# Optimization experiments

Measured on AMD Instinct MI355X. Metric: run time of the kernel, lower is better.

## Reference

```python
import jax, jax.numpy as jnp
from jax import lax
import numpy as np

# db6 decomposition low-pass filter (pywt convention)
_DB6_DEC_LO = np.array([
    -0.00107730108499558, 0.004777257511010651, 0.0005538422009938016,
    -0.031582039318031156, 0.02752286553001629, 0.09750160558707936,
    -0.12976686756709563, -0.22626469396516913, 0.3152503517092432,
    0.7511339080215775, 0.4946238903983854, 0.11154074335008017], dtype=np.float64)

def _make_filters():
    dec_lo = _DB6_DEC_LO
    rec_lo = dec_lo[::-1].copy()
    rec_hi = rec_lo[::-1].copy(); rec_hi[1::2] *= -1.0   # qmf(rec_lo)
    dec_hi = rec_hi[::-1].copy()
    # analysis implemented as correlation -> use time-reversed dec filters (= rec filters)
    a_lo = jnp.asarray(rec_lo, jnp.float32); a_hi = jnp.asarray(rec_hi, jnp.float32)
    # synthesis (conv_transpose) == correlation with flipped rec filters (= dec filters)
    s_lo = jnp.asarray(dec_lo, jnp.float32); s_hi = jnp.asarray(dec_hi, jnp.float32)
    return a_lo, a_hi, s_lo, s_hi

A_LO, A_HI, S_LO, S_HI = _make_filters()
FLEN = 12  # db6 filter length
LEVEL = 3

def _afb_last(x):
    """Analysis filter bank along last axis: symmetric pad + stride-2 correlation.
    x: [B,C,H,W] -> (lo, hi) each [B,C,H,outsize], outsize = floor((W+L-1)/2)."""
    B, C, H, W = x.shape
    outsize = (W + FLEN - 1) // 2
    p = 2 * (outsize - 1) - W + FLEN
    xp = jnp.pad(x, ((0, 0), (0, 0), (0, 0), (p // 2, (p + 1) // 2)), mode='symmetric')
    xr = xp.reshape(B * C * H, 1, xp.shape[-1])
    k = jnp.stack([A_LO, A_HI])[:, None, :]          # (2,1,L)
    y = lax.conv_general_dilated(xr, k, (2,), 'VALID')  # (BCH, 2, outsize)
    y = y.reshape(B, C, H, 2, outsize)
    return y[..., 0, :], y[..., 1, :]

def _sfb_last(lo, hi):
    """Synthesis filter bank along last axis via zero-upsampling + correlation.
    lo, hi: [B,C,H,n] -> [B,C,H,2n+2-L] (matches conv_transpose(stride=2, padding=L-2))."""
    B, C, H, n = lo.shape
    x2 = jnp.concatenate([lo.reshape(B * C * H, 1, n), hi.reshape(B * C * H, 1, n)], axis=1)
    k = jnp.stack([S_LO, S_HI])[None, :, :]          # (1,2,L)
    y = lax.conv_general_dilated(x2, k, (1,), [(1, 1)], lhs_dilation=(2,))
    return y.reshape(B, C, H, 2 * n + 2 - FLEN)

def _dwt2d(x):
    lo, hi = _afb_last(x)                            # along width
    llT, lhT = _afb_last(lo.swapaxes(-1, -2))        # along height
    hlT, hhT = _afb_last(hi.swapaxes(-1, -2))
    ll = llT.swapaxes(-1, -2)
    yh = jnp.stack([lhT.swapaxes(-1, -2), hlT.swapaxes(-1, -2), hhT.swapaxes(-1, -2)], axis=-1)
    return ll, yh                                    # ll [B,C,h,w], yh [B,C,h,w,3]

def _idwt2d(ll, yh):
    lh, hl, hh = yh[..., 0], yh[..., 1], yh[..., 2]
    ll = ll[..., :lh.shape[-2], :lh.shape[-1]]       # crop coarse ll to match highs
    lo = _sfb_last(ll.swapaxes(-1, -2), lh.swapaxes(-1, -2)).swapaxes(-1, -2)
    hi = _sfb_last(hl.swapaxes(-1, -2), hh.swapaxes(-1, -2)).swapaxes(-1, -2)
    return _sfb_last(lo, hi)

def _interp_bilinear(w, out_hw):
    """F.interpolate(mode='bilinear', align_corners=False) on [I,O,h,w] weights."""
    I, O, h, wd = w.shape
    Ho, Wo = int(out_hw[0]), int(out_hw[1])
    if (h, wd) == (Ho, Wo):
        return w
    ys = jnp.clip((jnp.arange(Ho, dtype=jnp.float32) + 0.5) * (h / Ho) - 0.5, 0.0, h - 1.0)
    xs = jnp.clip((jnp.arange(Wo, dtype=jnp.float32) + 0.5) * (wd / Wo) - 0.5, 0.0, wd - 1.0)
    y0 = jnp.floor(ys).astype(jnp.int32); y1 = jnp.minimum(y0 + 1, h - 1)
    x0 = jnp.floor(xs).astype(jnp.int32); x1 = jnp.minimum(x0 + 1, wd - 1)
    ty = (ys - y0)[:, None]; tx = xs - x0
    g = lambda yi, xi: w[:, :, yi, :][:, :, :, xi]
    top = g(y0, x0) * (1 - tx) + g(y0, x1) * tx
    bot = g(y1, x0) * (1 - tx) + g(y1, x1) * tx
    return top * (1 - ty) + bot * ty

def reference(x, weights):
    ll = x
    yh = []
    for _ in range(LEVEL):
        ll, h = _dwt2d(ll)
        yh.append(h)
    out_ll = jnp.einsum('bixy,ioxy->boxy', ll, _interp_bilinear(weights, ll.shape[-2:]))
    out_yh = [jnp.einsum('bixyz,ioxy->boxyz', h, _interp_bilinear(weights, h.shape[2:4])) for h in yh]
    y = out_ll
    for h in reversed(out_yh):
        y = _idwt2d(y, h)
    return y[:, :, :x.shape[2], :x.shape[3]]

def setup_inputs() -> dict:
    key = jax.random.key(0)
    k1, k2 = jax.random.split(key)
    B, Cin, Cout, H, W = 8, 64, 64, 256, 256
    x = jax.random.normal(k1, (B, Cin, H, W), dtype=jnp.float32)
    scale = 1.0 / (Cin * Cout)
    weights = scale * jax.random.uniform(k2, (Cin, Cout, 64, 64), dtype=jnp.float32)
    return {"x": x, "weights": weights}
```

## Files before the change

kernel.cpp:

```cpp
#include <hip/hip_runtime.h>

#define D0  -0.00107730108499558f
#define D1   0.004777257511010651f
#define D2   0.0005538422009938016f
#define D3  -0.031582039318031156f
#define D4   0.02752286553001629f
#define D5   0.09750160558707936f
#define D6  -0.12976686756709563f
#define D7  -0.22626469396516913f
#define D8   0.3152503517092432f
#define D9   0.7511339080215775f
#define D10  0.4946238903983854f
#define D11  0.11154074335008017f

__constant__ float c_ALO[12] = { D11, D10, D9, D8, D7, D6, D5, D4, D3, D2, D1, D0 };
__constant__ float c_AHI[12] = { D0, -D1, D2, -D3, D4, -D5, D6, -D7, D8, -D9, D10, -D11 };
__constant__ float c_SLO[12] = { D0, D1, D2, D3, D4, D5, D6, D7, D8, D9, D10, D11 };
__constant__ float c_SHI[12] = { -D11, D10, -D9, D8, -D7, D6, -D5, D4, -D3, D2, -D1, D0 };

#define NB 512

__device__ __forceinline__ void fma4(float4& a, const float4 v, const float c) {
  a.x = fmaf(v.x, c, a.x); a.y = fmaf(v.y, c, a.y);
  a.z = fmaf(v.z, c, a.z); a.w = fmaf(v.w, c, a.w);
}


__global__ __launch_bounds__(256) void k_afb_rows_nchw(
    const float* __restrict__ x, float4* __restrict__ lo, float4* __restrict__ hi) {
  __shared__ float lds[32][257];
  int h = blockIdx.x >> 4;
  int n0 = (blockIdx.x & 15) << 5;
  for (int idx = threadIdx.x; idx < 32 * 64; idx += 256) {
    int r = idx >> 6, c4 = idx & 63;
    float4 v = *(const float4*)(x + ((long)(n0 + r) * 256 + h) * 256 + (c4 << 2));
    int c = c4 << 2;
    lds[r][c] = v.x; lds[r][c + 1] = v.y; lds[r][c + 2] = v.z; lds[r][c + 3] = v.w;
  }
  __syncthreads();
  int nl4 = threadIdx.x & 7;
  int r0 = nl4 << 2;
  for (int k = threadIdx.x >> 3; k < 133; k += 32) {
    int base = 2 * k - 10;
    float4 aL = {0, 0, 0, 0}, aH = {0, 0, 0, 0};
#pragma unroll
    for (int t = 0; t < 12; ++t) {
      int j = base + t;
      j = (j < 0) ? (-j - 1) : ((j >= 256) ? (511 - j) : j);
      float v0 = lds[r0][j], v1 = lds[r0 + 1][j], v2 = lds[r0 + 2][j], v3 = lds[r0 + 3][j];
      float cl = c_ALO[t], ch = c_AHI[t];
      aL.x = fmaf(v0, cl, aL.x); aL.y = fmaf(v1, cl, aL.y);
      aL.z = fmaf(v2, cl, aL.z); aL.w = fmaf(v3, cl, aL.w);
      aH.x = fmaf(v0, ch, aH.x); aH.y = fmaf(v1, ch, aH.y);
      aH.z = fmaf(v2, ch, aH.z); aH.w = fmaf(v3, ch, aH.w);
    }
    long ob = ((long)h * 133 + k) * 128 + (n0 >> 2) + nl4;
    lo[ob] = aL;
    hi[ob] = aH;
  }
}

__global__ __launch_bounds__(256) void k_afb_rows_cl(
    const float4* __restrict__ in, float4* __restrict__ lo, float4* __restrict__ hi,
    int Win, int outW, int padL, int total) {
  int half = threadIdx.x >> 7, lane = threadIdx.x & 127;
  int p = blockIdx.x * 2 + half;
  if (p >= total) return;
  int h = p / outW, k = p - h * outW;
  int base = 2 * k - padL;
  const float4* rowb = in + (long)h * Win * 128;
  float4 aL = {0, 0, 0, 0}, aH = {0, 0, 0, 0};
#pragma unroll
  for (int t = 0; t < 12; ++t) {
    int j = base + t;
    j = (j < 0) ? (-j - 1) : ((j >= Win) ? (2 * Win - 1 - j) : j);
    float4 v = rowb[(long)j * 128 + lane];
    fma4(aL, v, c_ALO[t]);
    fma4(aH, v, c_AHI[t]);
  }
  long ob = (long)p * 128 + lane;
  lo[ob] = aL;
  hi[ob] = aH;
}

__global__ __launch_bounds__(256) void k_afb_cols_cl(
    const float4* __restrict__ in, float4* __restrict__ lo, float4* __restrict__ hi,
    int Hin, int W, int padL, int total) {
  int half = threadIdx.x >> 7, lane = threadIdx.x & 127;
  int p = blockIdx.x * 2 + half;
  if (p >= total) return;
  int k = p / W, w = p - k * W;
  int base = 2 * k - padL;
  long rstride = (long)W * 128;
  const float4* colb = in + (long)w * 128;
  float4 aL = {0, 0, 0, 0}, aH = {0, 0, 0, 0};
#pragma unroll
  for (int t = 0; t < 12; ++t) {
    int j = base + t;
    j = (j < 0) ? (-j - 1) : ((j >= Hin) ? (2 * Hin - 1 - j) : j);
    float4 v = colb[(long)j * rstride + lane];
    fma4(aL, v, c_ALO[t]);
    fma4(aH, v, c_AHI[t]);
  }
  long ob = (long)p * 128 + lane;
  lo[ob] = aL;
  hi[ob] = aH;
}


__global__ __launch_bounds__(256) void k_sfb_cols_cl(
    const float4* __restrict__ lo, long lors, const float4* __restrict__ hi, long hirs,
    float4* __restrict__ out, int n, int W, int total) {
  int half = threadIdx.x >> 7, lane = threadIdx.x & 127;
  int p = blockIdx.x * 2 + half;
  if (p >= total) return;
  int m = p / W, w = p - m * W;
  int t0 = 1 - (m & 1);
  const float4* lob = lo + (long)w * 128;
  const float4* hib = hi + (long)w * 128;
  float4 acc = {0, 0, 0, 0};
#pragma unroll
  for (int s6 = 0; s6 < 6; ++s6) {
    int t = t0 + 2 * s6;
    int j = (m + t - 1) >> 1;
    if (j >= 0 && j < n) {
      fma4(acc, lob[(long)j * lors + lane], c_SLO[t]);
      fma4(acc, hib[(long)j * hirs + lane], c_SHI[t]);
    }
  }
  out[(long)p * 128 + lane] = acc;
}

__global__ __launch_bounds__(256) void k_sfb_rows_cl(
    const float4* __restrict__ lo, long lors, const float4* __restrict__ hi, long hirs,
    float4* __restrict__ out, int n, int outW, int total) {
  int half = threadIdx.x >> 7, lane = threadIdx.x & 127;
  int p = blockIdx.x * 2 + half;
  if (p >= total) return;
  int h = p / outW, m = p - h * outW;
  int t0 = 1 - (m & 1);
  const float4* lob = lo + (long)h * lors;
  const float4* hib = hi + (long)h * hirs;
  float4 acc = {0, 0, 0, 0};
#pragma unroll
  for (int s6 = 0; s6 < 6; ++s6) {
    int t = t0 + 2 * s6;
    int j = (m + t - 1) >> 1;
    if (j >= 0 && j < n) {
      fma4(acc, lob[(long)j * 128 + lane], c_SLO[t]);
      fma4(acc, hib[(long)j * 128 + lane], c_SHI[t]);
    }
  }
  out[(long)p * 128 + lane] = acc;
}

__global__ __launch_bounds__(256) void k_sfb_rows_to_nchw(
    const float4* __restrict__ lo, const float4* __restrict__ hi, float4* __restrict__ out) {
  __shared__ float lds[32 * 257];
  int h = blockIdx.x >> 3;
  int m0 = (blockIdx.x & 7) << 5;
  const float4* lob = lo + (long)h * 133 * 128;
  const float4* hib = hi + (long)h * 133 * 128;
  for (int c = 0; c < 2; ++c) {
    int n04 = c << 6;
    for (int idx = threadIdx.x; idx < 32 * 64; idx += 256) {
      int ml = idx >> 6, nl4 = idx & 63;
      int m = m0 + ml;
      int t0 = 1 - (m & 1);
      float4 acc = {0, 0, 0, 0};
#pragma unroll
      for (int s6 = 0; s6 < 6; ++s6) {
        int t = t0 + 2 * s6;
        int j = (m + t - 1) >> 1;
        if (j >= 0 && j < 133) {
          fma4(acc, lob[(long)j * 128 + n04 + nl4], c_SLO[t]);
          fma4(acc, hib[(long)j * 128 + n04 + nl4], c_SHI[t]);
        }
      }
      int cb = ml * 257 + (nl4 << 2);
      lds[cb] = acc.x; lds[cb + 1] = acc.y; lds[cb + 2] = acc.z; lds[cb + 3] = acc.w;
    }
    __syncthreads();
    int ml4 = threadIdx.x & 7;
    for (int nl = threadIdx.x >> 3; nl < 256; nl += 32) {
      int nn = (c << 8) + nl;
      float4 v;
      v.x = lds[(ml4 * 4 + 0) * 257 + nl];
      v.y = lds[(ml4 * 4 + 1) * 257 + nl];
      v.z = lds[(ml4 * 4 + 2) * 257 + nl];
      v.w = lds[(ml4 * 4 + 3) * 257 + nl];
      out[((long)nn * 256 + h) * 64 + (m0 >> 2) + ml4] = v;
    }
    __syncthreads();
  }
}


__global__ __launch_bounds__(256) void k_transpose_w(
    const float* __restrict__ in, float* __restrict__ out) {
  __shared__ float tile[32][33];
  int bx = blockIdx.x & 127, by = blockIdx.x >> 7;
  int x0 = bx * 32, y0 = by * 32;
  int tx = threadIdx.x & 31, ty = threadIdx.x >> 5;
  for (int r = ty; r < 32; r += 8)
    tile[r][tx] = in[(long)(y0 + r) * 4096 + x0 + tx];
  __syncthreads();
  for (int r = ty; r < 32; r += 8)
    out[(long)(x0 + r) * 4096 + y0 + tx] = tile[tx][r];
}

__global__ __launch_bounds__(256) void k_mix(
    float* __restrict__ s0, float* __restrict__ s1, float* __restrict__ s2, float* __restrict__ s3,
    int nsub, const float* __restrict__ Wp, int Ho, int Wo) {
  __shared__ float Wm[4096];
  __shared__ float ins[NB];
  int p = blockIdx.x;
  int y = p / Wo, x = p - y * Wo;
  float sy = 64.0f / (float)Ho, sx = 64.0f / (float)Wo;
  float ys = fminf(fmaxf(((float)y + 0.5f) * sy - 0.5f, 0.0f), 63.0f);
  float xs = fminf(fmaxf(((float)x + 0.5f) * sx - 0.5f, 0.0f), 63.0f);
  int y0 = (int)ys, x0 = (int)xs;
  int y1 = min(y0 + 1, 63), x1 = min(x0 + 1, 63);
  float ty = ys - (float)y0, tx = xs - (float)x0;
  float w00 = (1.f - ty) * (1.f - tx), w01 = (1.f - ty) * tx;
  float w10 = ty * (1.f - tx), w11 = ty * tx;
  const float4* p00 = (const float4*)(Wp + (((long)y0 * 64 + x0) << 12));
  const float4* p01 = (const float4*)(Wp + (((long)y0 * 64 + x1) << 12));
  const float4* p10 = (const float4*)(Wp + (((long)y1 * 64 + x0) << 12));
  const float4* p11 = (const float4*)(Wp + (((long)y1 * 64 + x1) << 12));
  float4* Wm4 = (float4*)Wm;
  for (int t = threadIdx.x; t < 1024; t += 256) {
    float4 a = p00[t], b = p01[t], c = p10[t], d = p11[t];
    float4 r;
    r.x = w00 * a.x + w01 * b.x + w10 * c.x + w11 * d.x;
    r.y = w00 * a.y + w01 * b.y + w10 * c.y + w11 * d.y;
    r.z = w00 * a.z + w01 * b.z + w10 * c.z + w11 * d.z;
    r.w = w00 * a.w + w01 * b.w + w10 * c.w + w11 * d.w;
    Wm4[t] = r;
  }

  long pixoff = ((long)y * Wo + x) * NB;
  int bq = threadIdx.x >> 6;
  int o = threadIdx.x & 63;
  int b0 = bq * 2, b1 = b0 + 1;
  for (int s = 0; s < nsub; ++s) {
    float* base;
    if (s == 0) base = s0; else if (s == 1) base = s1; else if (s == 2) base = s2; else base = s3;
    base += pixoff;
    __syncthreads();
    if (threadIdx.x < 128)
      ((float4*)ins)[threadIdx.x] = ((const float4*)base)[threadIdx.x];
    __syncthreads();
    float a0 = 0.f, a1 = 0.f;
#pragma unroll 16
    for (int i = 0; i < 64; ++i) {
      float w = Wm[(i << 6) + o];
      a0 += ins[(b0 << 6) + i] * w;
      a1 += ins[(b1 << 6) + i] * w;
    }
    base[(b0 << 6) + o] = a0;
    base[(b1 << 6) + o] = a1;
  }
}


extern "C" void kernel_launch(void* const* d_in, const int* in_sizes, int n_in,
                              void* d_out, int out_size, void* d_ws, size_t ws_size,
                              hipStream_t stream) {
  const float* x = (const float*)d_in[0];
  const float* w = (const float*)d_in[1];
  float4* out = (float4*)d_out;
  float* ws = (float*)d_ws;

  float* T0  = ws;
  float* T1  = ws + 17432576;
  float* LL1 = ws + 34865152;
  float* LH1 = ws + 44058624;
  float* HL1 = ws + 53115392;
  float* HH1 = ws + 62172160;
  float* LL2 = ws + 71228928;
  float* LH2 = ws + 73883136;
  float* HL2 = ws + 76537344;
  float* HH2 = ws + 79191552;
  float* LL3 = ws + 81845760;
  float* LH3 = ws + 82706432;
  float* HL3 = ws + 83567104;
  float* HH3 = ws + 84427776;
  float* WP = T0;

#define F4(p) ((float4*)(p))
  dim3 blk(256);

  k_afb_rows_nchw<<<256 * 16, blk, 0, stream>>>(x, F4(T0), F4(T1));
  k_afb_cols_cl<<<(133 * 133 + 1) / 2, blk, 0, stream>>>(F4(T0), F4(LL1), F4(LH1), 256, 133, 10, 133 * 133);
  k_afb_cols_cl<<<(133 * 133 + 1) / 2, blk, 0, stream>>>(F4(T1), F4(HL1), F4(HH1), 256, 133, 10, 133 * 133);
  k_afb_rows_cl<<<(133 * 72 + 1) / 2, blk, 0, stream>>>(F4(LL1), F4(T0), F4(T1), 133, 72, 10, 133 * 72);
  k_afb_cols_cl<<<(72 * 72 + 1) / 2, blk, 0, stream>>>(F4(T0), F4(LL2), F4(LH2), 133, 72, 10, 72 * 72);
  k_afb_cols_cl<<<(72 * 72 + 1) / 2, blk, 0, stream>>>(F4(T1), F4(HL2), F4(HH2), 133, 72, 10, 72 * 72);
  k_afb_rows_cl<<<(72 * 41 + 1) / 2, blk, 0, stream>>>(F4(LL2), F4(T0), F4(T1), 72, 41, 10, 72 * 41);
  k_afb_cols_cl<<<(41 * 41 + 1) / 2, blk, 0, stream>>>(F4(T0), F4(LL3), F4(LH3), 72, 41, 10, 41 * 41);
  k_afb_cols_cl<<<(41 * 41 + 1) / 2, blk, 0, stream>>>(F4(T1), F4(HL3), F4(HH3), 72, 41, 10, 41 * 41);

  k_transpose_w<<<128 * 128, blk, 0, stream>>>(w, WP);

  k_mix<<<41 * 41, blk, 0, stream>>>(LL3, LH3, HL3, HH3, 4, WP, 41, 41);
  k_mix<<<72 * 72, blk, 0, stream>>>(LH2, HL2, HH2, nullptr, 3, WP, 72, 72);
  k_mix<<<133 * 133, blk, 0, stream>>>(LH1, HL1, HH1, nullptr, 3, WP, 133, 133);

  {
    float* C0 = T1;
    float* C1 = T1 + (long)72 * 41 * NB;
    k_sfb_cols_cl<<<(72 * 41 + 1) / 2, blk, 0, stream>>>(F4(LL3), 41 * 128, F4(LH3), 41 * 128, F4(C0), 41, 41, 72 * 41);
    k_sfb_cols_cl<<<(72 * 41 + 1) / 2, blk, 0, stream>>>(F4(HL3), 41 * 128, F4(HH3), 41 * 128, F4(C1), 41, 41, 72 * 41);
    k_sfb_rows_cl<<<(72 * 72 + 1) / 2, blk, 0, stream>>>(F4(C0), 41 * 128, F4(C1), 41 * 128, F4(LL2), 41, 72, 72 * 72);
  }
  {
    float* C0 = T1;
    float* C1 = T1 + (long)134 * 72 * NB;
    k_sfb_cols_cl<<<(134 * 72 + 1) / 2, blk, 0, stream>>>(F4(LL2), 72 * 128, F4(LH2), 72 * 128, F4(C0), 72, 72, 134 * 72);
    k_sfb_cols_cl<<<(134 * 72 + 1) / 2, blk, 0, stream>>>(F4(HL2), 72 * 128, F4(HH2), 72 * 128, F4(C1), 72, 72, 134 * 72);
    k_sfb_rows_cl<<<(134 * 134 + 1) / 2, blk, 0, stream>>>(F4(C0), 72 * 128, F4(C1), 72 * 128, F4(LL1), 72, 134, 134 * 134);
  }
  {
    k_sfb_cols_cl<<<(256 * 133 + 1) / 2, blk, 0, stream>>>(F4(LL1), 134 * 128, F4(LH1), 133 * 128, F4(T0), 133, 133, 256 * 133);
    k_sfb_cols_cl<<<(256 * 133 + 1) / 2, blk, 0, stream>>>(F4(HL1), 133 * 128, F4(HH1), 133 * 128, F4(T1), 133, 133, 256 * 133);
    k_sfb_rows_to_nchw<<<256 * 8, blk, 0, stream>>>(F4(T0), F4(T1), out);
  }
#undef F4
}
```

Measured before the change: 1.034 ms.

## Restructure channel-mix kernel: one subband per wavefront, XCD-aware block remap

The mix kernel now loads all subbands for a pixel into LDS at once and assigns one 64-thread group per subband, with each thread computing all 8 batches. This removes the per-subband barrier loop and reuses each weight read across 8 batches, with float4 input reads. Blocks are remapped so consecutive pixels land on the same XCD, which should improve L2 reuse of the interpolated weight corners. Block size drops to 192 for the 3-subband levels, trading occupancy shape and higher register use (8 accumulators) for less idle work.

Measured after the change: 1.047 ms. Within noise of the previous version (+1.2%).

```diff
diff --git a/kernel.cpp b/kernel.cpp
--- a/kernel.cpp
+++ b/kernel.cpp
@@ -213,8 +213,13 @@
     float* __restrict__ s0, float* __restrict__ s1, float* __restrict__ s2, float* __restrict__ s3,
     int nsub, const float* __restrict__ Wp, int Ho, int Wo) {
   __shared__ float Wm[4096];
-  __shared__ float ins[NB];
-  int p = blockIdx.x;
+  __shared__ float4 insLDS[4 * 128];
+
+  int nwg = Ho * Wo;
+  int q = nwg >> 3, r = nwg & 7;
+  int xcd = blockIdx.x & 7, idx = blockIdx.x >> 3;
+  int p = (xcd < r ? xcd * (q + 1) : r * (q + 1) + (xcd - r) * q) + idx;
+
   int y = p / Wo, x = p - y * Wo;
   float sy = 64.0f / (float)Ho, sx = 64.0f / (float)Wo;
   float ys = fminf(fmaxf(((float)y + 0.5f) * sy - 0.5f, 0.0f), 63.0f);
@@ -229,38 +234,55 @@
   const float4* p10 = (const float4*)(Wp + (((long)y1 * 64 + x0) << 12));
   const float4* p11 = (const float4*)(Wp + (((long)y1 * 64 + x1) << 12));
   float4* Wm4 = (float4*)Wm;
-  for (int t = threadIdx.x; t < 1024; t += 256) {
+  int nt = blockDim.x;
+  for (int t = threadIdx.x; t < 1024; t += nt) {
     float4 a = p00[t], b = p01[t], c = p10[t], d = p11[t];
-    float4 r;
-    r.x = w00 * a.x + w01 * b.x + w10 * c.x + w11 * d.x;
-    r.y = w00 * a.y + w01 * b.y + w10 * c.y + w11 * d.y;
-    r.z = w00 * a.z + w01 * b.z + w10 * c.z + w11 * d.z;
-    r.w = w00 * a.w + w01 * b.w + w10 * c.w + w11 * d.w;
-    Wm4[t] = r;
-  }
-
-  long pixoff = ((long)y * Wo + x) * NB;
-  int bq = threadIdx.x >> 6;
+    float4 rr;
+    rr.x = w00 * a.x + w01 * b.x + w10 * c.x + w11 * d.x;
+    rr.y = w00 * a.y + w01 * b.y + w10 * c.y + w11 * d.y;
+    rr.z = w00 * a.z + w01 * b.z + w10 * c.z + w11 * d.z;
+    rr.w = w00 * a.w + w01 * b.w + w10 * c.w + w11 * d.w;
+    Wm4[t] = rr;
+  }
+
+  long pixoff4 = (long)p * 128;
+  for (int s = 0; s < nsub; ++s) {
+    const float4* b4;
+    if (s == 0) b4 = (const float4*)s0; else if (s == 1) b4 = (const float4*)s1;
+    else if (s == 2) b4 = (const float4*)s2; else b4 = (const float4*)s3;
+    b4 += pixoff4;
+    for (int t = threadIdx.x; t < 128; t += nt) insLDS[(s << 7) + t] = b4[t];
+  }
+  __syncthreads();
+
+  int s = threadIdx.x >> 6;
   int o = threadIdx.x & 63;
-  int b0 = bq * 2, b1 = b0 + 1;
-  for (int s = 0; s < nsub; ++s) {
-    float* base;
-    if (s == 0) base = s0; else if (s == 1) base = s1; else if (s == 2) base = s2; else base = s3;
-    base += pixoff;
-    __syncthreads();
-    if (threadIdx.x < 128)
-      ((float4*)ins)[threadIdx.x] = ((const float4*)base)[threadIdx.x];
-    __syncthreads();
-    float a0 = 0.f, a1 = 0.f;
-#pragma unroll 16
-    for (int i = 0; i < 64; ++i) {
-      float w = Wm[(i << 6) + o];
-      a0 += ins[(b0 << 6) + i] * w;
-      a1 += ins[(b1 << 6) + i] * w;
-    }
-    base[(b0 << 6) + o] = a0;
-    base[(b1 << 6) + o] = a1;
-  }
+  float* base;
+  if (s == 0) base = s0; else if (s == 1) base = s1; else if (s == 2) base = s2; else base = s3;
+  base += pixoff4 * 4;
+
+  float acc[8] = {0.f, 0.f, 0.f, 0.f, 0.f, 0.f, 0.f, 0.f};
+  const float4* insS = insLDS + (s << 7);
+#pragma unroll 4
+  for (int i4 = 0; i4 < 16; ++i4) {
+    float w0 = Wm[((i4 << 2) + 0) * 64 + o];
+    float w1 = Wm[((i4 << 2) + 1) * 64 + o];
+    float w2 = Wm[((i4 << 2) + 2) * 64 + o];
+    float w3 = Wm[((i4 << 2) + 3) * 64 + o];
+#pragma unroll
+    for (int b = 0; b < 8; ++b) {
+      float4 iv = insS[(b << 4) + i4];
+      float a = acc[b];
+      a = fmaf(iv.x, w0, a);
+      a = fmaf(iv.y, w1, a);
+      a = fmaf(iv.z, w2, a);
+      a = fmaf(iv.w, w3, a);
+      acc[b] = a;
+    }
+  }
+#pragma unroll
+  for (int b = 0; b < 8; ++b)
+    base[(b << 6) + o] = acc[b];
 }
 
 
@@ -303,9 +325,9 @@
 
   k_transpose_w<<<128 * 128, blk, 0, stream>>>(w, WP);
 
-  k_mix<<<41 * 41, blk, 0, stream>>>(LL3, LH3, HL3, HH3, 4, WP, 41, 41);
-  k_mix<<<72 * 72, blk, 0, stream>>>(LH2, HL2, HH2, nullptr, 3, WP, 72, 72);
-  k_mix<<<133 * 133, blk, 0, stream>>>(LH1, HL1, HH1, nullptr, 3, WP, 133, 133);
+  k_mix<<<41 * 41, dim3(256), 0, stream>>>(LL3, LH3, HL3, HH3, 4, WP, 41, 41);
+  k_mix<<<72 * 72, dim3(192), 0, stream>>>(LH2, HL2, HH2, nullptr, 3, WP, 72, 72);
+  k_mix<<<133 * 133, dim3(192), 0, stream>>>(LH1, HL1, HH1, nullptr, 3, WP, 133, 133);
 
   {
     float* C0 = T1;
```
